# Kernel tuning notes

Measured on AMD Instinct MI355X. Metric: run time of the kernel, lower is better.

## Reference

```python
import jax, jax.numpy as jnp
import numpy as np

N_NODES = 50000
N_EDGES = 600000
IN_FEATS = 128
N_HIDDEN = 128
N_CLASSES = 40


def setup_inputs() -> dict:
    key = jax.random.key(0)
    ks = jax.random.split(key, 12)
    feat = jax.random.normal(ks[0], (N_NODES, IN_FEATS), dtype=jnp.float32)
    src = jax.random.randint(ks[1], (N_EDGES,), 0, N_NODES, dtype=jnp.int32)
    dst = jax.random.randint(ks[2], (N_EDGES,), 0, N_NODES, dtype=jnp.int32)
    dims = [(IN_FEATS, N_HIDDEN), (N_HIDDEN, N_HIDDEN), (N_HIDDEN, N_CLASSES)]
    params = {}
    for i, (di, do) in enumerate(dims):
        s = 1.0 / np.sqrt(di)
        params[f"w_self{i}"] = jax.random.uniform(ks[3 + 3 * i], (di, do), jnp.float32, -s, s)
        params[f"w_neigh{i}"] = jax.random.uniform(ks[4 + 3 * i], (di, do), jnp.float32, -s, s)
        params[f"b{i}"] = jnp.zeros((do,), jnp.float32)
    return dict(feat=feat, src=src, dst=dst, **params)


def _sage_layer(h, src, dst, w_self, w_neigh, b):
    # mean aggregation over in-neighbors: msg = h[src], reduce at dst
    msg_sum = jax.ops.segment_sum(h[src], dst, num_segments=N_NODES)  # [N, d]
    deg = jax.ops.segment_sum(jnp.ones((src.shape[0],), h.dtype), dst, num_segments=N_NODES)
    h_neigh = msg_sum / jnp.maximum(deg, 1.0)[:, None]
    # DGL SAGEConv(mean): out = fc_self(h) + fc_neigh(mean_neigh) + bias
    return h @ w_self + h_neigh @ w_neigh + b


def reference(feat, src, dst,
              w_self0, w_neigh0, b0,
              w_self1, w_neigh1, b1,
              w_self2, w_neigh2, b2):
    # dropout p=0.0 -> identity
    h = _sage_layer(feat, src, dst, w_self0, w_neigh0, b0)
    h = jax.nn.relu(h)
    h = _sage_layer(h, src, dst, w_self1, w_neigh1, b1)
    h = jax.nn.relu(h)
    h = _sage_layer(h, src, dst, w_self2, w_neigh2, b2)
    return h
```

## Files before the change

### kernel.cpp

```cpp
#include <hip/hip_runtime.h>

#define N_NODES 50000
#define N_EDGES 600000

typedef short bf16x8 __attribute__((ext_vector_type(8)));
typedef float f32x4  __attribute__((ext_vector_type(4)));
typedef unsigned short u16x8 __attribute__((ext_vector_type(8)));
typedef unsigned short u16x4 __attribute__((ext_vector_type(4)));

__device__ inline ushort rne_bf16(float a) {
    union { float f; unsigned u; } v; v.f = a;
    return (ushort)((v.u + 0x7FFFu + ((v.u >> 16) & 1u)) >> 16);
}
__device__ inline float bf16_to_f32(ushort h) {
    return __uint_as_float((unsigned)h << 16);
}
__device__ inline void split_bf16(float a, ushort& hi, ushort& lo) {
    hi = rne_bf16(a);
    float hv = bf16_to_f32(hi);
    lo = rne_bf16(a - hv);
}


__global__ void count_deg_kernel(const int* __restrict__ dst, int* __restrict__ deg, int ne) {
    int e = blockIdx.x * blockDim.x + threadIdx.x;
    if (e < ne) atomicAdd(&deg[dst[e]], 1);
}

__global__ __launch_bounds__(256) void block_sums_kernel(const int* __restrict__ deg,
                                                         int* __restrict__ bsum, int n) {
    __shared__ int s[256];
    int t = threadIdx.x;
    int i = blockIdx.x * 256 + t;
    s[t] = (i < n) ? deg[i] : 0;
    __syncthreads();
    #pragma unroll
    for (int d = 128; d > 0; d >>= 1) {
        if (t < d) s[t] += s[t + d];
        __syncthreads();
    }
    if (t == 0) bsum[blockIdx.x] = s[0];
}

__global__ __launch_bounds__(256) void scatter_fused_kernel(const int* __restrict__ deg,
                                                            const int* __restrict__ bsum,
                                                            int* __restrict__ off,
                                                            int* __restrict__ cur,
                                                            int n, int nb) {
    __shared__ int s[256];
    int t = threadIdx.x;

    int bv = (t < nb) ? bsum[t] : 0;
    s[t] = bv;
    __syncthreads();
    #pragma unroll
    for (int d = 1; d < 256; d <<= 1) {
        int x = (t >= d) ? s[t - d] : 0;
        __syncthreads();
        s[t] += x;
        __syncthreads();
    }
    int base = (blockIdx.x > 0) ? s[blockIdx.x - 1] : 0;
    if (blockIdx.x == 0 && t == 0) off[n] = s[255];
    __syncthreads();

    int i = blockIdx.x * 256 + t;
    int v = (i < n) ? deg[i] : 0;
    s[t] = v;
    __syncthreads();
    #pragma unroll
    for (int d = 1; d < 256; d <<= 1) {
        int x = (t >= d) ? s[t - d] : 0;
        __syncthreads();
        s[t] += x;
        __syncthreads();
    }
    if (i < n) {
        int excl = s[t] - v + base;
        off[i] = excl;
        cur[i] = excl;
    }
}

__global__ void fill_csr_kernel(const int* __restrict__ src, const int* __restrict__ dst,
                                int* __restrict__ cur, int* __restrict__ ssrc, int ne) {
    int e = blockIdx.x * blockDim.x + threadIdx.x;
    if (e < ne) {
        int p = atomicAdd(&cur[dst[e]], 1);
        ssrc[p] = src[e];
    }
}

__global__ void convert_all_w(const float* __restrict__ ws0, const float* __restrict__ wn0,
                              const float* __restrict__ ws1, const float* __restrict__ wn1,
                              const float* __restrict__ ws2, const float* __restrict__ wn2,
                              ushort* __restrict__ Bth0, ushort* __restrict__ Btl0,
                              ushort* __restrict__ Bth1, ushort* __restrict__ Btl1,
                              ushort* __restrict__ Bth2, ushort* __restrict__ Btl2) {
    int b = blockIdx.x;
    int k = threadIdx.x;
    const float *Ws, *Wn;
    ushort *H, *L;
    int dout, n;
    if (b < 256)      { n = b;       dout = 128; Ws = ws0; Wn = wn0; H = Bth0; L = Btl0; }
    else if (b < 512) { n = b - 256; dout = 128; Ws = ws1; Wn = wn1; H = Bth1; L = Btl1; }
    else              { n = b - 512; dout = 40;  Ws = ws2; Wn = wn2; H = Bth2; L = Btl2; }
    float w = (n < dout) ? Ws[(long)k * dout + n] : Wn[(long)k * dout + (n - dout)];
    ushort hi, lo;
    split_bf16(w, hi, lo);
    H[n * 128 + k] = hi;
    L[n * 128 + k] = lo;
}


#define KDIM 128
#define APAD 136

__device__ inline void stage_a32(const float* __restrict__ A, int bm, int M, int tid,
                                 ushort* __restrict__ Ahi, ushort* __restrict__ Alo) {
    const int m   = tid >> 3;
    const int seg = (tid & 7) * 16;
    const int grow = bm + m;
    float f[16];
    if (grow < M) {
        const float* ap = A + (long)grow * KDIM + seg;
        #pragma unroll
        for (int q = 0; q < 4; ++q) {
            float4 a = *(const float4*)(ap + q * 4);
            f[q * 4 + 0] = a.x; f[q * 4 + 1] = a.y;
            f[q * 4 + 2] = a.z; f[q * 4 + 3] = a.w;
        }
    } else {
        #pragma unroll
        for (int i = 0; i < 16; ++i) f[i] = 0.f;
    }
    ushort h[16], l[16];
    #pragma unroll
    for (int i = 0; i < 16; ++i) split_bf16(f[i], h[i], l[i]);
    #pragma unroll
    for (int q = 0; q < 2; ++q) {
        uint4 hw, lw;
        hw.x = (unsigned)h[q*8+0] | ((unsigned)h[q*8+1] << 16);
        hw.y = (unsigned)h[q*8+2] | ((unsigned)h[q*8+3] << 16);
        hw.z = (unsigned)h[q*8+4] | ((unsigned)h[q*8+5] << 16);
        hw.w = (unsigned)h[q*8+6] | ((unsigned)h[q*8+7] << 16);
        lw.x = (unsigned)l[q*8+0] | ((unsigned)l[q*8+1] << 16);
        lw.y = (unsigned)l[q*8+2] | ((unsigned)l[q*8+3] << 16);
        lw.z = (unsigned)l[q*8+4] | ((unsigned)l[q*8+5] << 16);
        lw.w = (unsigned)l[q*8+6] | ((unsigned)l[q*8+7] << 16);
        *(uint4*)&Ahi[m * APAD + seg + q * 8] = hw;
        *(uint4*)&Alo[m * APAD + seg + q * 8] = lw;
    }
}

__global__ __launch_bounds__(256, 3) void gemm_mfma_wide(
    const float* __restrict__ A,
    const ushort* __restrict__ Bth, const ushort* __restrict__ Btl,
    const float* __restrict__ bias,
    float* __restrict__ S, ushort* __restrict__ T, int M)
{
    __shared__ ushort Ahi[32 * APAD];
    __shared__ ushort Alo[32 * APAD];

    const int tid = threadIdx.x;
    const int wave = tid >> 6;
    const int lane = tid & 63;
    const int lane16 = lane & 15;
    const int quad = lane >> 4;
    const int half = blockIdx.x & 1;
    const int colbase = half * 128 + wave * 32;
    const int ntiles = (M + 31) >> 5;

    bf16x8 Bh[4][2], Bl[4][2];
    #pragma unroll
    for (int c = 0; c < 4; ++c) {
        #pragma unroll
        for (int ct = 0; ct < 2; ++ct) {
            const long boff = (long)(colbase + 16 * ct + lane16) * KDIM + c * 32 + quad * 8;
            Bh[c][ct] = *(const bf16x8*)(Bth + boff);
            Bl[c][ct] = *(const bf16x8*)(Btl + boff);
        }
    }

    for (int rt = blockIdx.x >> 1; rt < ntiles; rt += gridDim.x >> 1) {
        const int bm = rt * 32;
        __syncthreads();
        stage_a32(A, bm, M, tid, Ahi, Alo);
        __syncthreads();

        f32x4 acc[2][2] = {};

        #pragma unroll
        for (int c = 0; c < 4; ++c) {
            const int k0 = c * 32 + quad * 8;
            bf16x8 ah[2], al[2];
            #pragma unroll
            for (int r = 0; r < 2; ++r) {
                int off = (16 * r + lane16) * APAD + k0;
                ah[r] = *(const bf16x8*)&Ahi[off];
                al[r] = *(const bf16x8*)&Alo[off];
            }
            #pragma unroll
            for (int ct = 0; ct < 2; ++ct) {
                #pragma unroll
                for (int r = 0; r < 2; ++r) {
                    acc[r][ct] = __builtin_amdgcn_mfma_f32_16x16x32_bf16(Bh[c][ct], ah[r], acc[r][ct], 0, 0, 0);
                    acc[r][ct] = __builtin_amdgcn_mfma_f32_16x16x32_bf16(Bl[c][ct], ah[r], acc[r][ct], 0, 0, 0);
                    acc[r][ct] = __builtin_amdgcn_mfma_f32_16x16x32_bf16(Bh[c][ct], al[r], acc[r][ct], 0, 0, 0);
                }
            }
        }

        #pragma unroll
        for (int ct = 0; ct < 2; ++ct) {
            const int colL = wave * 32 + 16 * ct + quad * 4;
            #pragma unroll
            for (int r = 0; r < 2; ++r) {
                const int row = bm + 16 * r + lane16;
                if (row < M) {
                    if (half == 0) {
                        f32x4 bv = *(const f32x4*)(bias + colL);
                        *(f32x4*)(S + (long)row * 128 + colL) = acc[r][ct] + bv;
                    } else {
                        u16x4 t4;
                        #pragma unroll
                        for (int i = 0; i < 4; ++i) t4[i] = rne_bf16(acc[r][ct][i]);
                        *(u16x4*)(T + (long)row * 128 + colL) = t4;
                    }
                }
            }
        }
    }
}

__global__ __launch_bounds__(256, 4) void gemm_mfma_narrow(
    const float* __restrict__ A,
    const ushort* __restrict__ Bth, const ushort* __restrict__ Btl,
    const float* __restrict__ bias,
    float* __restrict__ S, ushort* __restrict__ T, int M)
{
    __shared__ ushort Ahi[32 * APAD];
    __shared__ ushort Alo[32 * APAD];

    const int tid = threadIdx.x;
    const int wave = tid >> 6;
    const int lane = tid & 63;
    const int lane16 = lane & 15;
    const int quad = lane >> 4;
    const int bm = blockIdx.x * 32;

    const int rt = wave & 1;
    const int cg = wave >> 1;
    const int ctbase = cg * 3;
    const int nct = cg ? 2 : 3;

    stage_a32(A, bm, M, tid, Ahi, Alo);
    __syncthreads();

    f32x4 acc[3] = {};

    #pragma unroll
    for (int c = 0; c < 4; ++c) {
        const int off = (rt * 16 + lane16) * APAD + c * 32 + quad * 8;
        bf16x8 ah = *(const bf16x8*)&Ahi[off];
        bf16x8 al = *(const bf16x8*)&Alo[off];
        #pragma unroll
        for (int j = 0; j < 3; ++j) {
            if (j < nct) {
                const int ct = ctbase + j;
                const long boff = (long)(16 * ct + lane16) * KDIM + c * 32 + quad * 8;
                bf16x8 bh = *(const bf16x8*)(Bth + boff);
                bf16x8 bl = *(const bf16x8*)(Btl + boff);
                acc[j] = __builtin_amdgcn_mfma_f32_16x16x32_bf16(bh, ah, acc[j], 0, 0, 0);
                acc[j] = __builtin_amdgcn_mfma_f32_16x16x32_bf16(bl, ah, acc[j], 0, 0, 0);
                acc[j] = __builtin_amdgcn_mfma_f32_16x16x32_bf16(bh, al, acc[j], 0, 0, 0);
            }
        }
    }

    #pragma unroll
    for (int j = 0; j < 3; ++j) {
        if (j < nct) {
            const int ct = ctbase + j;
            const int col0 = 16 * ct + quad * 4;
            const bool toS = col0 < 40;
            const int row = bm + rt * 16 + lane16;
            if (row < M) {
                if (toS) {
                    f32x4 bv = *(const f32x4*)(bias + col0);
                    *(f32x4*)(S + (long)row * 40 + col0) = acc[j] + bv;
                } else {
                    u16x4 t4;
                    #pragma unroll
                    for (int i = 0; i < 4; ++i) t4[i] = rne_bf16(acc[j][i]);
                    *(u16x4*)(T + (long)row * 40 + (col0 - 40)) = t4;
                }
            }
        }
    }
}


template <int RELU>
__global__ __launch_bounds__(256) void agg128_kernel(
    const float* __restrict__ S, const ushort* __restrict__ T,
    const int* __restrict__ off, const int* __restrict__ ssrc,
    float* __restrict__ out, int nnodes)
{
    const int node = (blockIdx.x * 256 + threadIdx.x) >> 6;
    if (node >= nnodes) return;
    const int lane = threadIdx.x & 63;
    const int slot = lane >> 4;
    const int col8 = (lane & 15) * 8;

    const int a = off[node];
    const int b = off[node + 1];

    f32x4 acc0a = {0,0,0,0}, acc0b = {0,0,0,0};
    f32x4 acc1a = {0,0,0,0}, acc1b = {0,0,0,0};

    int i = a;
    for (; i + 8 <= b; i += 8) {
        int s0 = ssrc[i + slot];
        int s1 = ssrc[i + 4 + slot];
        u16x8 v0 = *(const u16x8*)(T + (long)s0 * 128 + col8);
        u16x8 v1 = *(const u16x8*)(T + (long)s1 * 128 + col8);
        #pragma unroll
        for (int j = 0; j < 4; ++j) {
            acc0a[j] += bf16_to_f32(v0[j]);
            acc0b[j] += bf16_to_f32(v0[4 + j]);
            acc1a[j] += bf16_to_f32(v1[j]);
            acc1b[j] += bf16_to_f32(v1[4 + j]);
        }
    }
    for (; i < b; i += 4) {
        int e = i + slot;
        if (e < b) {
            int s = ssrc[e];
            u16x8 v = *(const u16x8*)(T + (long)s * 128 + col8);
            #pragma unroll
            for (int j = 0; j < 4; ++j) {
                acc0a[j] += bf16_to_f32(v[j]);
                acc0b[j] += bf16_to_f32(v[4 + j]);
            }
        }
    }
    f32x4 accA = acc0a + acc1a;
    f32x4 accB = acc0b + acc1b;

    #pragma unroll
    for (int m = 16; m <= 32; m <<= 1) {
        #pragma unroll
        for (int j = 0; j < 4; ++j) {
            accA[j] += __shfl_xor((float)accA[j], m);
            accB[j] += __shfl_xor((float)accB[j], m);
        }
    }

    if (slot == 0) {
        int deg = b - a;
        float scale = (deg > 0) ? (1.0f / (float)deg) : 0.f;
        f32x4 sA = *(const f32x4*)(S + (long)node * 128 + col8);
        f32x4 sB = *(const f32x4*)(S + (long)node * 128 + col8 + 4);
        f32x4 rA = sA + accA * scale;
        f32x4 rB = sB + accB * scale;
        if (RELU) {
            #pragma unroll
            for (int j = 0; j < 4; ++j) {
                rA[j] = fmaxf(rA[j], 0.f);
                rB[j] = fmaxf(rB[j], 0.f);
            }
        }
        *(f32x4*)(out + (long)node * 128 + col8) = rA;
        *(f32x4*)(out + (long)node * 128 + col8 + 4) = rB;
    }
}

template <int RELU>
__global__ __launch_bounds__(256) void agg40_kernel(
    const float* __restrict__ S, const ushort* __restrict__ T,
    const int* __restrict__ off, const int* __restrict__ ssrc,
    float* __restrict__ out, int nnodes)
{
    const int node = (blockIdx.x * 256 + threadIdx.x) >> 6;
    if (node >= nnodes) return;
    const int lane = threadIdx.x & 63;
    const bool active = lane < 60;
    const int slot = active ? (lane / 10) : 5;
    const int fi = lane % 10;
    const int fo = fi * 4;

    const int a = off[node];
    const int b = off[node + 1];

    f32x4 acc0 = {0,0,0,0}, acc1 = {0,0,0,0};

    int i = a;
    for (; i + 12 <= b; i += 12) {
        int s0 = ssrc[i + slot];
        int s1 = ssrc[i + 6 + slot];
        u16x4 v0 = *(const u16x4*)(T + (long)s0 * 40 + fo);
        u16x4 v1 = *(const u16x4*)(T + (long)s1 * 40 + fo);
        if (active) {
            #pragma unroll
            for (int j = 0; j < 4; ++j) {
                acc0[j] += bf16_to_f32(v0[j]);
                acc1[j] += bf16_to_f32(v1[j]);
            }
        }
    }
    for (; i < b; i += 6) {
        int e = i + slot;
        if (active && e < b) {
            int s = ssrc[e];
            u16x4 v = *(const u16x4*)(T + (long)s * 40 + fo);
            #pragma unroll
            for (int j = 0; j < 4; ++j) acc0[j] += bf16_to_f32(v[j]);
        }
    }
    f32x4 acc = acc0 + acc1;

    f32x4 tot = acc;
    #pragma unroll
    for (int d = 10; d <= 50; d += 10) {
        int srcl = fi + d;
        #pragma unroll
        for (int j = 0; j < 4; ++j) tot[j] += __shfl((float)acc[j], srcl);
    }

    if (lane < 10) {
        int deg = b - a;
        float scale = (deg > 0) ? (1.0f / (float)deg) : 0.f;
        f32x4 s4 = *(const f32x4*)(S + (long)node * 40 + fo);
        f32x4 r = s4 + tot * scale;
        if (RELU) {
            #pragma unroll
            for (int j = 0; j < 4; ++j) r[j] = fmaxf(r[j], 0.f);
        }
        *(f32x4*)(out + (long)node * 40 + fo) = r;
    }
}


extern "C" void kernel_launch(void* const* d_in, const int* in_sizes, int n_in,
                              void* d_out, int out_size, void* d_ws, size_t ws_size,
                              hipStream_t stream) {
    const float* feat = (const float*)d_in[0];
    const int*   src  = (const int*)d_in[1];
    const int*   dst  = (const int*)d_in[2];
    const float* ws0  = (const float*)d_in[3];
    const float* wn0  = (const float*)d_in[4];
    const float* b0   = (const float*)d_in[5];
    const float* ws1  = (const float*)d_in[6];
    const float* wn1  = (const float*)d_in[7];
    const float* b1   = (const float*)d_in[8];
    const float* ws2  = (const float*)d_in[9];
    const float* wn2  = (const float*)d_in[10];
    const float* b2   = (const float*)d_in[11];

    const int N = N_NODES;
    const int NE = N_EDGES;
    const int NB = (N + 255) / 256;

    char* ws = (char*)d_ws;
    int*    offsets = (int*)(ws + 0);
    int*    cursor  = (int*)(ws + 200704);
    int*    degi    = (int*)(ws + 401408);
    int*    bsum    = (int*)(ws + 601600);
    int*    ssrc    = (int*)(ws + 603648);
    ushort* Bth0 = (ushort*)(ws + 200704);
    ushort* Btl0 = (ushort*)(ws + 266240);
    ushort* Bth1 = (ushort*)(ws + 331776);
    ushort* Btl1 = (ushort*)(ws + 397312);
    ushort* Bth2 = (ushort*)(ws + 462848);
    ushort* Btl2 = (ushort*)(ws + 483328);
    float*  hbuf = (float*)(ws + 3003904);
    float*  sbuf = (float*)(ws + 28603904);
    ushort* tbuf = (ushort*)(ws + 54203904);

    hipMemsetAsync(degi, 0, (size_t)N * sizeof(int), stream);
    count_deg_kernel<<<(NE + 255) / 256, 256, 0, stream>>>(dst, degi, NE);
    block_sums_kernel<<<NB, 256, 0, stream>>>(degi, bsum, N);
    scatter_fused_kernel<<<NB, 256, 0, stream>>>(degi, bsum, offsets, cursor, N, NB);
    fill_csr_kernel<<<(NE + 255) / 256, 256, 0, stream>>>(src, dst, cursor, ssrc, NE);

    convert_all_w<<<592, 128, 0, stream>>>(ws0, wn0, ws1, wn1, ws2, wn2,
                                           Bth0, Btl0, Bth1, Btl1, Bth2, Btl2);

    const int ntiles = (N + 31) / 32;
    const int gw = 2 * ntiles;
    const int gn = ntiles;
    const int ga = (N + 3) / 4;

    gemm_mfma_wide<<<gw, 256, 0, stream>>>(feat, Bth0, Btl0, b0, sbuf, tbuf, N);
    agg128_kernel<1><<<ga, 256, 0, stream>>>(sbuf, tbuf, offsets, ssrc, hbuf, N);

    gemm_mfma_wide<<<gw, 256, 0, stream>>>(hbuf, Bth1, Btl1, b1, sbuf, tbuf, N);
    agg128_kernel<1><<<ga, 256, 0, stream>>>(sbuf, tbuf, offsets, ssrc, hbuf, N);

    gemm_mfma_narrow<<<gn, 256, 0, stream>>>(hbuf, Bth2, Btl2, b2, sbuf, tbuf, N);
    agg40_kernel<0><<<ga, 256, 0, stream>>>(sbuf, tbuf, offsets, ssrc, (float*)d_out, N);
}
```

Measured before the change: 326.0 us.

## Double-buffer A tiles and use persistent grids in MFMA GEMM kernels

```diff
diff --git a/kernel.cpp b/kernel.cpp
--- a/kernel.cpp
+++ b/kernel.cpp
@@ -116,12 +116,8 @@
 #define KDIM 128
 #define APAD 136
 
-__device__ inline void stage_a32(const float* __restrict__ A, int bm, int M, int tid,
-                                 ushort* __restrict__ Ahi, ushort* __restrict__ Alo) {
-    const int m   = tid >> 3;
-    const int seg = (tid & 7) * 16;
-    const int grow = bm + m;
-    float f[16];
+__device__ inline void load_a16(const float* __restrict__ A, int grow, int M, int seg,
+                                float* __restrict__ f) {
     if (grow < M) {
         const float* ap = A + (long)grow * KDIM + seg;
         #pragma unroll
@@ -134,6 +130,11 @@
         #pragma unroll
         for (int i = 0; i < 16; ++i) f[i] = 0.f;
     }
+}
+
+__device__ inline void split_store16(const float* __restrict__ f,
+                                     ushort* __restrict__ Ahi, ushort* __restrict__ Alo,
+                                     int m, int seg) {
     ushort h[16], l[16];
     #pragma unroll
     for (int i = 0; i < 16; ++i) split_bf16(f[i], h[i], l[i]);
@@ -159,8 +160,8 @@
     const float* __restrict__ bias,
     float* __restrict__ S, ushort* __restrict__ T, int M)
 {
-    __shared__ ushort Ahi[32 * APAD];
-    __shared__ ushort Alo[32 * APAD];
+    __shared__ ushort AhiB[2][32 * APAD];
+    __shared__ ushort AloB[2][32 * APAD];
 
     const int tid = threadIdx.x;
     const int wave = tid >> 6;
@@ -170,6 +171,9 @@
     const int half = blockIdx.x & 1;
     const int colbase = half * 128 + wave * 32;
     const int ntiles = (M + 31) >> 5;
+    const int bstride = gridDim.x >> 1;
+    const int m   = tid >> 3;
+    const int seg = (tid & 7) * 16;
 
     bf16x8 Bh[4][2], Bl[4][2];
     #pragma unroll
@@ -181,24 +185,40 @@
             Bl[c][ct] = *(const bf16x8*)(Btl + boff);
         }
     }
-
-    for (int rt = blockIdx.x >> 1; rt < ntiles; rt += gridDim.x >> 1) {
-        const int bm = rt * 32;
-        __syncthreads();
-        stage_a32(A, bm, M, tid, Ahi, Alo);
-        __syncthreads();
+    f32x4 bv[2] = {};
+    if (half == 0) {
+        #pragma unroll
+        for (int ct = 0; ct < 2; ++ct)
+            bv[ct] = *(const f32x4*)(bias + wave * 32 + 16 * ct + quad * 4);
+    }
+
+    int rt = blockIdx.x >> 1;
+    if (rt >= ntiles) return;
+
+    float fa[16];
+    load_a16(A, rt * 32 + m, M, seg, fa);
+    split_store16(fa, &AhiB[0][0], &AloB[0][0], m, seg);
+    __syncthreads();
+
+    int cur = 0;
+    while (true) {
+        const int nrt = rt + bstride;
+        float fn[16];
+        if (nrt < ntiles) load_a16(A, nrt * 32 + m, M, seg, fn);
+
+        const ushort* AH = &AhiB[cur][0];
+        const ushort* AL = &AloB[cur][0];
 
         f32x4 acc[2][2] = {};
-
         #pragma unroll
         for (int c = 0; c < 4; ++c) {
             const int k0 = c * 32 + quad * 8;
             bf16x8 ah[2], al[2];
             #pragma unroll
             for (int r = 0; r < 2; ++r) {
-                int off = (16 * r + lane16) * APAD + k0;
-                ah[r] = *(const bf16x8*)&Ahi[off];
-                al[r] = *(const bf16x8*)&Alo[off];
+                const int off = (16 * r + lane16) * APAD + k0;
+                ah[r] = *(const bf16x8*)&AH[off];
+                al[r] = *(const bf16x8*)&AL[off];
             }
             #pragma unroll
             for (int ct = 0; ct < 2; ++ct) {
@@ -216,11 +236,10 @@
             const int colL = wave * 32 + 16 * ct + quad * 4;
             #pragma unroll
             for (int r = 0; r < 2; ++r) {
-                const int row = bm + 16 * r + lane16;
+                const int row = rt * 32 + 16 * r + lane16;
                 if (row < M) {
                     if (half == 0) {
-                        f32x4 bv = *(const f32x4*)(bias + colL);
-                        *(f32x4*)(S + (long)row * 128 + colL) = acc[r][ct] + bv;
+                        *(f32x4*)(S + (long)row * 128 + colL) = acc[r][ct] + bv[ct];
                     } else {
                         u16x4 t4;
                         #pragma unroll
@@ -230,65 +249,91 @@
                 }
             }
         }
-    }
-}
-
-__global__ __launch_bounds__(256, 4) void gemm_mfma_narrow(
+
+        if (nrt >= ntiles) break;
+        split_store16(fn, &AhiB[cur ^ 1][0], &AloB[cur ^ 1][0], m, seg);
+        __syncthreads();
+        cur ^= 1;
+        rt = nrt;
+    }
+}
+
+__global__ __launch_bounds__(256, 2) void gemm_mfma_narrow(
     const float* __restrict__ A,
     const ushort* __restrict__ Bth, const ushort* __restrict__ Btl,
     const float* __restrict__ bias,
     float* __restrict__ S, ushort* __restrict__ T, int M)
 {
-    __shared__ ushort Ahi[32 * APAD];
-    __shared__ ushort Alo[32 * APAD];
+    __shared__ ushort AhiB[2][32 * APAD];
+    __shared__ ushort AloB[2][32 * APAD];
 
     const int tid = threadIdx.x;
     const int wave = tid >> 6;
     const int lane = tid & 63;
     const int lane16 = lane & 15;
     const int quad = lane >> 4;
-    const int bm = blockIdx.x * 32;
-
-    const int rt = wave & 1;
+    const int rtw = wave & 1;
     const int cg = wave >> 1;
     const int ctbase = cg * 3;
     const int nct = cg ? 2 : 3;
-
-    stage_a32(A, bm, M, tid, Ahi, Alo);
-    __syncthreads();
-
-    f32x4 acc[3] = {};
-
+    const int ntiles = (M + 31) >> 5;
+    const int m   = tid >> 3;
+    const int seg = (tid & 7) * 16;
+
+    bf16x8 Bh[4][3], Bl[4][3];
     #pragma unroll
     for (int c = 0; c < 4; ++c) {
-        const int off = (rt * 16 + lane16) * APAD + c * 32 + quad * 8;
-        bf16x8 ah = *(const bf16x8*)&Ahi[off];
-        bf16x8 al = *(const bf16x8*)&Alo[off];
         #pragma unroll
         for (int j = 0; j < 3; ++j) {
             if (j < nct) {
-                const int ct = ctbase + j;
-                const long boff = (long)(16 * ct + lane16) * KDIM + c * 32 + quad * 8;
-                bf16x8 bh = *(const bf16x8*)(Bth + boff);
-                bf16x8 bl = *(const bf16x8*)(Btl + boff);
-                acc[j] = __builtin_amdgcn_mfma_f32_16x16x32_bf16(bh, ah, acc[j], 0, 0, 0);
-                acc[j] = __builtin_amdgcn_mfma_f32_16x16x32_bf16(bl, ah, acc[j], 0, 0, 0);
-                acc[j] = __builtin_amdgcn_mfma_f32_16x16x32_bf16(bh, al, acc[j], 0, 0, 0);
-            }
-        }
-    }
-
-    #pragma unroll
-    for (int j = 0; j < 3; ++j) {
-        if (j < nct) {
-            const int ct = ctbase + j;
-            const int col0 = 16 * ct + quad * 4;
-            const bool toS = col0 < 40;
-            const int row = bm + rt * 16 + lane16;
-            if (row < M) {
-                if (toS) {
-                    f32x4 bv = *(const f32x4*)(bias + col0);
-                    *(f32x4*)(S + (long)row * 40 + col0) = acc[j] + bv;
+                const long boff = (long)(16 * (ctbase + j) + lane16) * KDIM + c * 32 + quad * 8;
+                Bh[c][j] = *(const bf16x8*)(Bth + boff);
+                Bl[c][j] = *(const bf16x8*)(Btl + boff);
+            }
+        }
+    }
+
+    int rt = blockIdx.x;
+    if (rt >= ntiles) return;
+
+    float fa[16];
+    load_a16(A, rt * 32 + m, M, seg, fa);
+    split_store16(fa, &AhiB[0][0], &AloB[0][0], m, seg);
+    __syncthreads();
+
+    int cur = 0;
+    while (true) {
+        const int nrt = rt + gridDim.x;
+        float fn[16];
+        if (nrt < ntiles) load_a16(A, nrt * 32 + m, M, seg, fn);
+
+        const ushort* AH = &AhiB[cur][0];
+        const ushort* AL = &AloB[cur][0];
+
+        f32x4 acc[3] = {};
+        #pragma unroll
+        for (int c = 0; c < 4; ++c) {
+            const int off = (rtw * 16 + lane16) * APAD + c * 32 + quad * 8;
+            bf16x8 ah = *(const bf16x8*)&AH[off];
+            bf16x8 al = *(const bf16x8*)&AL[off];
+            #pragma unroll
+            for (int j = 0; j < 3; ++j) {
+                if (j < nct) {
+                    acc[j] = __builtin_amdgcn_mfma_f32_16x16x32_bf16(Bh[c][j], ah, acc[j], 0, 0, 0);
+                    acc[j] = __builtin_amdgcn_mfma_f32_16x16x32_bf16(Bl[c][j], ah, acc[j], 0, 0, 0);
+                    acc[j] = __builtin_amdgcn_mfma_f32_16x16x32_bf16(Bh[c][j], al, acc[j], 0, 0, 0);
+                }
+            }
+        }
+
+        const int row = rt * 32 + rtw * 16 + lane16;
+        #pragma unroll
+        for (int j = 0; j < 3; ++j) {
+            if (j < nct && row < M) {
+                const int col0 = 16 * (ctbase + j) + quad * 4;
+                if (col0 < 40) {
+                    f32x4 bvv = *(const f32x4*)(bias + col0);
+                    *(f32x4*)(S + (long)row * 40 + col0) = acc[j] + bvv;
                 } else {
                     u16x4 t4;
                     #pragma unroll
@@ -297,6 +342,12 @@
                 }
             }
         }
+
+        if (nrt >= ntiles) break;
+        split_store16(fn, &AhiB[cur ^ 1][0], &AloB[cur ^ 1][0], m, seg);
+        __syncthreads();
+        cur ^= 1;
+        rt = nrt;
     }
 }
 
@@ -487,9 +538,8 @@
     convert_all_w<<<592, 128, 0, stream>>>(ws0, wn0, ws1, wn1, ws2, wn2,
                                            Bth0, Btl0, Bth1, Btl1, Bth2, Btl2);
 
-    const int ntiles = (N + 31) / 32;
-    const int gw = 2 * ntiles;
-    const int gn = ntiles;
+    const int gw = 768;
+    const int gn = 512;
     const int ga = (N + 3) / 4;
 
     gemm_mfma_wide<<<gw, 256, 0, stream>>>(feat, Bth0, Btl0, b0, sbuf, tbuf, N);
```

Measured after the change: 290.0 us. -11.0%, faster.
